# Optimization experiments

Measured on AMD Instinct MI355X. Metric: run time of the kernel, lower is better.

## Reference

```python
import jax, jax.numpy as jnp
import numpy as np

B, N, F = 2048, 65536, 128
NUM_K = 3
NUM_LABELS = 10
EXPONENT = 2.0


def setup_inputs() -> dict:
    key = jax.random.key(0)
    k1, k2, k3 = jax.random.split(key, 3)
    # positive inputs: tf.pow with a float exponent NaNs on negative bases
    x_input = jax.random.uniform(k1, (B, F), dtype=jnp.float32)
    train_inputs = jax.random.uniform(k2, (N, F), dtype=jnp.float32)
    train_labels = jax.random.randint(k3, (N,), 0, NUM_LABELS, dtype=jnp.int32)
    features = jnp.ones((F,), dtype=jnp.float32)  # abe_features, ones init
    return {
        "x_input": x_input,
        "train_inputs": train_inputs,
        "train_labels": train_labels,
        "features": features,
    }


def reference(x_input, train_inputs, train_labels, features):
    # weighted_inputs = features * train_inputs
    w = features[None, :] * train_inputs  # [N, F]

    # Minkowsky distance (faithful to the TF graph):
    # (sum(x^p) + sum(w^p))^(1/p) - 2 * x @ w^T
    left = jnp.sum(x_input ** EXPONENT, axis=1)[:, None]   # [B, 1]
    right = jnp.sum(w ** EXPONENT, axis=1)[None, :]        # [1, N]
    distance = (left + right) ** (1.0 / EXPONENT) - 2.0 * (x_input @ w.T)  # [B, N]

    # top-k nearest neighbors via top_k of negated distances
    values, indices = jax.lax.top_k(-distance, NUM_K)      # [B, K]

    # gather neighbor labels and average (tf.reduce_mean on int = floor div)
    labels = train_labels[indices]                          # [B, K] int32
    outputs = jnp.sum(labels, axis=1) // NUM_K              # [B] int32
    one_hot = jax.nn.one_hot(outputs, NUM_LABELS, dtype=jnp.float32)  # [B, NUM_LABELS]

    return (one_hot, values, indices, labels)
```

## Files before the change

### kernel.cpp

```cpp
#include <hip/hip_runtime.h>
#include <hip/hip_bf16.h>
#include <cstdint>
#include <cstddef>

typedef short bf16x8 __attribute__((ext_vector_type(8)));
typedef float f32x4 __attribute__((ext_vector_type(4)));

namespace {
constexpr int kB = 2048;
constexpr int kN = 65536;
constexpr int kF = 128;
constexpr int kLabels = 10;
constexpr int kIMax = 0x7fffffff;

constexpr int BCOLS = 128;
constexpr int PROWS = 128;
constexpr int NPANEL = kB / PROWS;
constexpr int NCH = 4;
constexpr int NG = NPANEL * NCH;
constexpr int NSUB = kN / 16;
constexpr float kMargin = 0.25f;
}

#define TOP3_INSERT(dd, ii, D0, I0, D1, I1, D2, I2)                              \
  do {                                                                           \
    float _d = (dd); int _i = (ii);                                              \
    if (_d < (D0) || (_d == (D0) && _i < (I0))) {                                \
      (D2) = (D1); (I2) = (I1); (D1) = (D0); (I1) = (I0); (D0) = _d; (I0) = _i;  \
    } else if (_d < (D1) || (_d == (D1) && _i < (I1))) {                         \
      (D2) = (D1); (I2) = (I1); (D1) = _d; (I1) = _i;                            \
    } else if (_d < (D2) || (_d == (D2) && _i < (I2))) {                         \
      (D2) = _d; (I2) = _i;                                                      \
    }                                                                            \
  } while (0)

__device__ inline unsigned short f2bf(float a) {
  __hip_bfloat16 h = __float2bfloat16(a);
  return __builtin_bit_cast(unsigned short, h);
}

__device__ inline void gload_lds16(const void* g, void* l) {
  __builtin_amdgcn_global_load_lds(
      (const __attribute__((address_space(1))) void*)g,
      (__attribute__((address_space(3))) void*)l, 16, 0, 0);
}

__global__ __launch_bounds__(256) void pack_sumsq_kernel(
    const float* __restrict__ x, const float* __restrict__ train,
    const float* __restrict__ features, unsigned short* __restrict__ Ap,
    unsigned short* __restrict__ Bp, float* __restrict__ left,
    float* __restrict__ right) {
  const int wid = (int)((blockIdx.x * 256 + threadIdx.x) >> 6);
  const int lane = threadIdx.x & 63;
  if (wid >= kB + kN) return;
  const float2 fv = reinterpret_cast<const float2*>(features)[lane];
  const float* src;
  unsigned short* dst;
  float pm0, pm1, sm0, sm1;
  if (wid < kB) {
    src = x + (size_t)wid * kF;
    dst = Ap + (size_t)wid * 128;
    pm0 = fv.x; pm1 = fv.y;
    sm0 = 1.0f; sm1 = 1.0f;
  } else {
    src = train + (size_t)(wid - kB) * kF;
    dst = Bp + (size_t)(wid - kB) * 128;
    pm0 = 1.0f; pm1 = 1.0f;
    sm0 = fv.x; sm1 = fv.y;
  }
  const float2 v = reinterpret_cast<const float2*>(src)[lane];
  const float pa = v.x * pm0, pb = v.y * pm1;
  const float sa = v.x * sm0, sb = v.y * sm1;
  const unsigned short ha = f2bf(pa), hb = f2bf(pb);
  reinterpret_cast<unsigned int*>(dst)[lane] = (unsigned int)ha | ((unsigned int)hb << 16);
  float s = sa * sa + sb * sb;
  #pragma unroll
  for (int m = 1; m <= 32; m <<= 1) s += __shfl_xor(s, m);
  if (lane == 0) {
    if (wid < kB) left[wid] = s;
    else right[wid - kB] = s;
  }
}

__global__ __launch_bounds__(256, 2) void knn_main_kernel(
    const unsigned short* __restrict__ Ap, const unsigned short* __restrict__ Bp,
    const float* __restrict__ left, const float* __restrict__ right,
    float* __restrict__ minbuf) {
  __shared__ alignas(16) unsigned short lsB[NCH * BCOLS * 32];
  __shared__ alignas(16) unsigned short lsA[3][PROWS * 32];
  __shared__ float lsL[kB];
  __shared__ float lsR[BCOLS];

  const int slice = blockIdx.x;
  const int col0 = slice * BCOLS;
  const int t = threadIdx.x;
  const int lane = t & 63;
  const int wm = (t >> 6) >> 1;
  const int wn = (t >> 6) & 1;

  #pragma unroll
  for (int i = 0; i < 2; ++i)
    reinterpret_cast<float4*>(lsL)[t + i * 256] =
        reinterpret_cast<const float4*>(left)[t + i * 256];
  if (t < BCOLS / 4)
    reinterpret_cast<float4*>(lsR)[t] =
        reinterpret_cast<const float4*>(right + col0)[t];

  const int rr = t >> 2;
  const int p = t & 3;
  size_t aoff[2], boff[2];
  int ldsoff[2];
  #pragma unroll
  for (int i = 0; i < 2; ++i) {
    const int r = i * 64 + rr;
    const int ps = p ^ ((r >> 1) & 3);
    aoff[i] = (size_t)r * 256 + (size_t)ps * 16;
    boff[i] = (size_t)(col0 + r) * 256 + (size_t)ps * 16;
    ldsoff[i] = i * 4096 + t * 16;
  }

  int offA[2], offB[4];
  #pragma unroll
  for (int mf = 0; mf < 4; ++mf) {
    if (mf < 2) {}
  }
  int offAf[4], offBf[4];
  #pragma unroll
  for (int mf = 0; mf < 4; ++mf) {
    const int rl = wm * 64 + mf * 16 + (lane & 15);
    offAf[mf] = rl * 64 + (((lane >> 4) ^ ((rl >> 1) & 3)) * 16);
  }
  #pragma unroll
  for (int nf = 0; nf < 4; ++nf) {
    const int cl = wn * 64 + nf * 16 + (lane & 15);
    offBf[nf] = cl * 64 + (((lane >> 4) ^ ((cl >> 1) & 3)) * 16);
  }

  const char* ApB = (const char*)Ap;
  const char* BpB = (const char*)Bp;

  auto stageA = [&](int buf, int g) {
    const int mp = g >> 2, c = g & 3;
    char* lA = (char*)&lsA[buf][0];
    #pragma unroll
    for (int i = 0; i < 2; ++i)
      gload_lds16(ApB + aoff[i] + (size_t)mp * 32768 + (size_t)c * 64,
                  lA + ldsoff[i]);
  };

  {
    char* lB = (char*)&lsB[0];
    #pragma unroll
    for (int c = 0; c < NCH; ++c)
      #pragma unroll
      for (int i = 0; i < 2; ++i)
        gload_lds16(BpB + boff[i] + (size_t)c * 64, lB + c * 8192 + ldsoff[i]);
  }
  stageA(0, 0);
  stageA(1, 1);
  __syncthreads();

  float rj[4];
  #pragma unroll
  for (int nf = 0; nf < 4; ++nf)
    rj[nf] = lsR[wn * 64 + nf * 16 + (lane & 15)];

  const bool bwriter = (lane & 3) == 0;
  const int subbase = slice * 8 + wn * 4 + ((lane >> 2) & 3);

  for (int mp = 0; mp < NPANEL; ++mp) {
    f32x4 acc[4][4];
    #pragma unroll
    for (int mf = 0; mf < 4; ++mf)
      #pragma unroll
      for (int nf = 0; nf < 4; ++nf)
        acc[mf][nf] = (f32x4){0.f, 0.f, 0.f, 0.f};

    for (int c = 0; c < NCH; ++c) {
      const int g = mp * 4 + c;
      if (g < NG - 2) stageA((g + 2) % 3, g + 2);
      if (g < NG - 2)       asm volatile("s_waitcnt vmcnt(4)" ::: "memory");
      else if (g == NG - 2) asm volatile("s_waitcnt vmcnt(2)" ::: "memory");
      else                  asm volatile("s_waitcnt vmcnt(0)" ::: "memory");
      __builtin_amdgcn_s_barrier();
      asm volatile("" ::: "memory");

      const char* lA = (const char*)&lsA[g % 3][0];
      const char* lB = (const char*)&lsB[c * 4096 * 2 / 2];
      lB = (const char*)&lsB[0] + c * 8192;
      bf16x8 a[4], b[4];
      #pragma unroll
      for (int mf = 0; mf < 4; ++mf)
        a[mf] = *reinterpret_cast<const bf16x8*>(lA + offAf[mf]);
      #pragma unroll
      for (int nf = 0; nf < 4; ++nf)
        b[nf] = *reinterpret_cast<const bf16x8*>(lB + offBf[nf]);
      __builtin_amdgcn_s_setprio(1);
      #pragma unroll
      for (int mf = 0; mf < 4; ++mf)
        #pragma unroll
        for (int nf = 0; nf < 4; ++nf)
          acc[mf][nf] = __builtin_amdgcn_mfma_f32_16x16x32_bf16(
              a[mf], b[nf], acc[mf][nf], 0, 0, 0);
      __builtin_amdgcn_s_setprio(0);
      asm volatile("" ::: "memory");
      __builtin_amdgcn_s_barrier();
      asm volatile("" ::: "memory");
    }

    const int prow0 = mp * PROWS + wm * 64;
    #pragma unroll
    for (int mf = 0; mf < 4; ++mf) {
      #pragma unroll
      for (int rg = 0; rg < 4; ++rg) {
        const int row = prow0 + mf * 16 + (lane >> 4) * 4 + rg;
        const float l = lsL[row];
        float d0 = sqrtf(l + rj[0]) - 2.0f * acc[mf][0][rg];
        float d1 = sqrtf(l + rj[1]) - 2.0f * acc[mf][1][rg];
        float d2 = sqrtf(l + rj[2]) - 2.0f * acc[mf][2][rg];
        float d3 = sqrtf(l + rj[3]) - 2.0f * acc[mf][3][rg];
        float v = fminf(fminf(d0, d1), fminf(d2, d3));
        v = fminf(v, __shfl_xor(v, 1));
        v = fminf(v, __shfl_xor(v, 2));
        if (bwriter)
          minbuf[(size_t)row * NSUB + subbase] = v;
      }
    }
  }
}

__global__ __launch_bounds__(256) void select_rescore_kernel(
    const float* __restrict__ x, const float* __restrict__ train,
    const float* __restrict__ features, const float* __restrict__ left,
    const float* __restrict__ right, const int* __restrict__ labels,
    const float* __restrict__ minbuf, float* __restrict__ out) {
  __shared__ float Xs[4][kF];
  const int t = threadIdx.x;
  if (t < 128) {
    const int rr = t >> 5, q = t & 31;
    float4 xv = reinterpret_cast<const float4*>(
        x + (size_t)(blockIdx.x * 4 + rr) * kF)[q];
    const float4 f = reinterpret_cast<const float4*>(features)[q];
    xv.x *= f.x; xv.y *= f.y; xv.z *= f.z; xv.w *= f.w;
    reinterpret_cast<float4*>(&Xs[rr][0])[q] = xv;
  }
  __syncthreads();
  const int wave = t >> 6, lane = t & 63;
  const int row = blockIdx.x * 4 + wave;
  const float lr = left[row];
  const float* mrow = minbuf + (size_t)row * NSUB;

  float v0 = __builtin_inff(), v1 = v0, v2 = v0;
  #pragma unroll 4
  for (int i = 0; i < NSUB / 64; ++i) {
    const float m = mrow[i * 64 + lane];
    if (m < v0) { v2 = v1; v1 = v0; v0 = m; }
    else if (m < v1) { v2 = v1; v1 = m; }
    else if (m < v2) { v2 = m; }
  }
  #pragma unroll
  for (int msk = 1; msk <= 32; msk <<= 1) {
    const float e0 = __shfl_xor(v0, msk), e1 = __shfl_xor(v1, msk), e2 = __shfl_xor(v2, msk);
    if (e0 < v0) { v2 = v1; v1 = v0; v0 = e0; } else if (e0 < v1) { v2 = v1; v1 = e0; } else if (e0 < v2) v2 = e0;
    if (e1 < v0) { v2 = v1; v1 = v0; v0 = e1; } else if (e1 < v1) { v2 = v1; v1 = e1; } else if (e1 < v2) v2 = e1;
    if (e2 < v0) { v2 = v1; v1 = v0; v0 = e2; } else if (e2 < v1) { v2 = v1; v1 = e2; } else if (e2 < v2) v2 = e2;
  }
  const float tau = v2 + kMargin;

  float d0 = __builtin_inff(), d1 = d0, d2 = d0;
  int i0 = kIMax, i1 = kIMax, i2 = kIMax;
  for (int base = 0; base < NSUB; base += 64) {
    const float m = mrow[base + lane];
    unsigned long long msk = __ballot(m <= tau);
    while (msk) {
      const int bpos = __builtin_ctzll(msk);
      msk &= msk - 1;
      const int sub = base + bpos;
      if (lane < 16) {
        const int j = (sub >> 3) * 128 + ((sub >> 2) & 1) * 64 +
                      (lane >> 2) * 16 + (sub & 3) * 4 + (lane & 3);
        const float4* wp = reinterpret_cast<const float4*>(train + (size_t)j * kF);
        float acc = 0.f;
        #pragma unroll 8
        for (int kq = 0; kq < 32; ++kq) {
          const float4 w4 = wp[kq];
          const float4 x4 = reinterpret_cast<const float4*>(&Xs[wave][0])[kq];
          acc = fmaf(x4.w, w4.w, fmaf(x4.z, w4.z, fmaf(x4.y, w4.y, fmaf(x4.x, w4.x, acc))));
        }
        const float d = sqrtf(lr + right[j]) - 2.0f * acc;
        TOP3_INSERT(d, j, d0, i0, d1, i1, d2, i2);
      }
    }
  }
  #pragma unroll
  for (int msk = 1; msk <= 32; msk <<= 1) {
    const float e0 = __shfl_xor(d0, msk), e1 = __shfl_xor(d1, msk), e2 = __shfl_xor(d2, msk);
    const int f0 = __shfl_xor(i0, msk), f1 = __shfl_xor(i1, msk), f2 = __shfl_xor(i2, msk);
    TOP3_INSERT(e0, f0, d0, i0, d1, i1, d2, i2);
    TOP3_INSERT(e1, f1, d0, i0, d1, i1, d2, i2);
    TOP3_INSERT(e2, f2, d0, i0, d1, i1, d2, i2);
  }
  if (lane == 0) {
    const int l0 = labels[i0], l1 = labels[i1], l2 = labels[i2];
    const int o = (l0 + l1 + l2) / 3;
    float* one_hot = out;
    float* values = out + (size_t)kB * kLabels;
    float* indices = values + (size_t)kB * 3;
    float* labs = indices + (size_t)kB * 3;
    #pragma unroll
    for (int c = 0; c < kLabels; ++c)
      one_hot[(size_t)row * kLabels + c] = (c == o) ? 1.0f : 0.0f;
    values[row * 3 + 0] = -d0; values[row * 3 + 1] = -d1; values[row * 3 + 2] = -d2;
    indices[row * 3 + 0] = (float)i0; indices[row * 3 + 1] = (float)i1; indices[row * 3 + 2] = (float)i2;
    labs[row * 3 + 0] = (float)l0; labs[row * 3 + 1] = (float)l1; labs[row * 3 + 2] = (float)l2;
  }
}

extern "C" void kernel_launch(void* const* d_in, const int* in_sizes, int n_in,
                              void* d_out, int out_size, void* d_ws, size_t ws_size,
                              hipStream_t stream) {
  const float* x = (const float*)d_in[0];
  const float* train = (const float*)d_in[1];
  const int* labels = (const int*)d_in[2];
  const float* features = (const float*)d_in[3];
  float* out = (float*)d_out;

  char* ws = (char*)d_ws;
  unsigned short* Bp = (unsigned short*)ws;
  unsigned short* Ap = (unsigned short*)(ws + 16777216);
  float* left = (float*)(ws + 17301504);
  float* right = (float*)(ws + 17309696);
  float* minbuf = (float*)(ws + 17571840);

  pack_sumsq_kernel<<<((kB + kN) * 64 + 255) / 256, 256, 0, stream>>>(
      x, train, features, Ap, Bp, left, right);
  knn_main_kernel<<<kN / BCOLS, 256, 0, stream>>>(Ap, Bp, left, right, minbuf);
  select_rescore_kernel<<<kB / 4, 256, 0, stream>>>(
      x, train, features, left, right, labels, minbuf, out);
}
```

Before: 284.5 us.

## Hold B fragments in registers and read A directly from global memory

Drops the LDS staging pipeline for both operands. The B tile for the block's column slice is loaded once into registers (16 bf16x8 fragments per lane), and A fragments are read straight from global memory (or L2) into registers each chunk, with no barriers inside the panel loop. This removes the LDS traffic, the async-copy wait counts and the per-chunk barriers. In exchange it increases register pressure and gives up cross-wave sharing of A loads, so each wave issues its own redundant global reads and the memory latency is no longer explicitly pipelined.

```diff
diff --git a/kernel.cpp b/kernel.cpp
--- a/kernel.cpp
+++ b/kernel.cpp
@@ -17,7 +17,6 @@
 constexpr int PROWS = 128;
 constexpr int NPANEL = kB / PROWS;
 constexpr int NCH = 4;
-constexpr int NG = NPANEL * NCH;
 constexpr int NSUB = kN / 16;
 constexpr float kMargin = 0.25f;
 }
@@ -37,12 +36,6 @@
 __device__ inline unsigned short f2bf(float a) {
   __hip_bfloat16 h = __float2bfloat16(a);
   return __builtin_bit_cast(unsigned short, h);
-}
-
-__device__ inline void gload_lds16(const void* g, void* l) {
-  __builtin_amdgcn_global_load_lds(
-      (const __attribute__((address_space(1))) void*)g,
-      (__attribute__((address_space(3))) void*)l, 16, 0, 0);
 }
 
 __global__ __launch_bounds__(256) void pack_sumsq_kernel(
@@ -86,10 +79,7 @@
     const unsigned short* __restrict__ Ap, const unsigned short* __restrict__ Bp,
     const float* __restrict__ left, const float* __restrict__ right,
     float* __restrict__ minbuf) {
-  __shared__ alignas(16) unsigned short lsB[NCH * BCOLS * 32];
-  __shared__ alignas(16) unsigned short lsA[3][PROWS * 32];
   __shared__ float lsL[kB];
-  __shared__ float lsR[BCOLS];
 
   const int slice = blockIdx.x;
   const int col0 = slice * BCOLS;
@@ -102,73 +92,37 @@
   for (int i = 0; i < 2; ++i)
     reinterpret_cast<float4*>(lsL)[t + i * 256] =
         reinterpret_cast<const float4*>(left)[t + i * 256];
-  if (t < BCOLS / 4)
-    reinterpret_cast<float4*>(lsR)[t] =
-        reinterpret_cast<const float4*>(right + col0)[t];
-
-  const int rr = t >> 2;
-  const int p = t & 3;
-  size_t aoff[2], boff[2];
-  int ldsoff[2];
-  #pragma unroll
-  for (int i = 0; i < 2; ++i) {
-    const int r = i * 64 + rr;
-    const int ps = p ^ ((r >> 1) & 3);
-    aoff[i] = (size_t)r * 256 + (size_t)ps * 16;
-    boff[i] = (size_t)(col0 + r) * 256 + (size_t)ps * 16;
-    ldsoff[i] = i * 4096 + t * 16;
-  }
-
-  int offA[2], offB[4];
-  #pragma unroll
-  for (int mf = 0; mf < 4; ++mf) {
-    if (mf < 2) {}
-  }
-  int offAf[4], offBf[4];
-  #pragma unroll
-  for (int mf = 0; mf < 4; ++mf) {
-    const int rl = wm * 64 + mf * 16 + (lane & 15);
-    offAf[mf] = rl * 64 + (((lane >> 4) ^ ((rl >> 1) & 3)) * 16);
-  }
-  #pragma unroll
-  for (int nf = 0; nf < 4; ++nf) {
-    const int cl = wn * 64 + nf * 16 + (lane & 15);
-    offBf[nf] = cl * 64 + (((lane >> 4) ^ ((cl >> 1) & 3)) * 16);
-  }
+  __syncthreads();
+
+  float rj[4];
+  #pragma unroll
+  for (int nf = 0; nf < 4; ++nf)
+    rj[nf] = right[col0 + wn * 64 + nf * 16 + (lane & 15)];
+
+  const char* BpB = (const char*)Bp;
+  bf16x8 bfr[4][4];
+  #pragma unroll
+  for (int c = 0; c < 4; ++c)
+    #pragma unroll
+    for (int nf = 0; nf < 4; ++nf) {
+      const size_t addr =
+          (size_t)(col0 + wn * 64 + nf * 16 + (lane & 15)) * 256 +
+          (size_t)c * 64 + (size_t)(lane >> 4) * 16;
+      bfr[c][nf] = *reinterpret_cast<const bf16x8*>(BpB + addr);
+    }
 
   const char* ApB = (const char*)Ap;
-  const char* BpB = (const char*)Bp;
-
-  auto stageA = [&](int buf, int g) {
-    const int mp = g >> 2, c = g & 3;
-    char* lA = (char*)&lsA[buf][0];
-    #pragma unroll
-    for (int i = 0; i < 2; ++i)
-      gload_lds16(ApB + aoff[i] + (size_t)mp * 32768 + (size_t)c * 64,
-                  lA + ldsoff[i]);
-  };
-
-  {
-    char* lB = (char*)&lsB[0];
-    #pragma unroll
-    for (int c = 0; c < NCH; ++c)
-      #pragma unroll
-      for (int i = 0; i < 2; ++i)
-        gload_lds16(BpB + boff[i] + (size_t)c * 64, lB + c * 8192 + ldsoff[i]);
-  }
-  stageA(0, 0);
-  stageA(1, 1);
-  __syncthreads();
-
-  float rj[4];
-  #pragma unroll
-  for (int nf = 0; nf < 4; ++nf)
-    rj[nf] = lsR[wn * 64 + nf * 16 + (lane & 15)];
+  size_t abase[4];
+  #pragma unroll
+  for (int mf = 0; mf < 4; ++mf)
+    abase[mf] = (size_t)(wm * 64 + mf * 16 + (lane & 15)) * 256 +
+                (size_t)(lane >> 4) * 16;
 
   const bool bwriter = (lane & 3) == 0;
   const int subbase = slice * 8 + wn * 4 + ((lane >> 2) & 3);
 
   for (int mp = 0; mp < NPANEL; ++mp) {
+    const size_t poff = (size_t)mp * (PROWS * 256);
     f32x4 acc[4][4];
     #pragma unroll
     for (int mf = 0; mf < 4; ++mf)
@@ -176,36 +130,21 @@
       for (int nf = 0; nf < 4; ++nf)
         acc[mf][nf] = (f32x4){0.f, 0.f, 0.f, 0.f};
 
+    #pragma unroll
     for (int c = 0; c < NCH; ++c) {
-      const int g = mp * 4 + c;
-      if (g < NG - 2) stageA((g + 2) % 3, g + 2);
-      if (g < NG - 2)       asm volatile("s_waitcnt vmcnt(4)" ::: "memory");
-      else if (g == NG - 2) asm volatile("s_waitcnt vmcnt(2)" ::: "memory");
-      else                  asm volatile("s_waitcnt vmcnt(0)" ::: "memory");
-      __builtin_amdgcn_s_barrier();
-      asm volatile("" ::: "memory");
-
-      const char* lA = (const char*)&lsA[g % 3][0];
-      const char* lB = (const char*)&lsB[c * 4096 * 2 / 2];
-      lB = (const char*)&lsB[0] + c * 8192;
-      bf16x8 a[4], b[4];
+      bf16x8 a[4];
       #pragma unroll
       for (int mf = 0; mf < 4; ++mf)
-        a[mf] = *reinterpret_cast<const bf16x8*>(lA + offAf[mf]);
-      #pragma unroll
-      for (int nf = 0; nf < 4; ++nf)
-        b[nf] = *reinterpret_cast<const bf16x8*>(lB + offBf[nf]);
+        a[mf] = *reinterpret_cast<const bf16x8*>(
+            ApB + abase[mf] + poff + (size_t)c * 64);
       __builtin_amdgcn_s_setprio(1);
       #pragma unroll
       for (int mf = 0; mf < 4; ++mf)
         #pragma unroll
         for (int nf = 0; nf < 4; ++nf)
           acc[mf][nf] = __builtin_amdgcn_mfma_f32_16x16x32_bf16(
-              a[mf], b[nf], acc[mf][nf], 0, 0, 0);
+              a[mf], bfr[c][nf], acc[mf][nf], 0, 0, 0);
       __builtin_amdgcn_s_setprio(0);
-      asm volatile("" ::: "memory");
-      __builtin_amdgcn_s_barrier();
-      asm volatile("" ::: "memory");
     }
 
     const int prow0 = mp * PROWS + wm * 64;
```

Result: no change. 285.6 us (+0.4%).
